# Optimization experiments

Hardware: AMD Instinct MI355X
Metric: run time of the kernel (lower is better)

Reference implementation:

```python
import jax, jax.numpy as jnp
import numpy as np

MAX_RHO = 12.0
N_THETAS = 16
N_RHOS = 5
G = N_THETAS * N_RHOS          # 80 gaussians
W_NUM = 5                      # weights_num == n_feat -> per-channel conv
OUT_DIM = 80                   # conv_shape = [80, 80]
EPS = 1e-5


def _initial_coords():
    grid_rho = np.linspace(0.0, MAX_RHO, num=N_RHOS + 1)[1:]
    grid_theta = np.linspace(0.0, 2.0 * np.pi, num=N_THETAS + 1)[:-1]
    gr, gt = np.meshgrid(grid_rho, grid_theta, sparse=False)
    return gr.T.flatten().astype(np.float32), gt.T.flatten().astype(np.float32)


def setup_inputs() -> dict:
    key = jax.random.key(0)
    ks = jax.random.split(key, 6)
    B, N, V = 2, 500, 64
    input_feat = jax.random.normal(ks[0], (B, N, V, W_NUM), dtype=jnp.float32)
    rho_coords = jax.random.uniform(ks[1], (B, N, V), dtype=jnp.float32) * MAX_RHO
    theta_coords = jax.random.uniform(ks[2], (B, N, V), dtype=jnp.float32) * (2.0 * np.pi)
    mask = (jax.random.uniform(ks[3], (B, N, V, 1)) > 0.2).astype(jnp.float32)

    mu_r0, mu_t0 = _initial_coords()
    mu_rho = jnp.tile(jnp.asarray(mu_r0)[None, :], (W_NUM, 1))       # [W, G]
    mu_theta = jnp.tile(jnp.asarray(mu_t0)[None, :], (W_NUM, 1))     # [W, G]
    sigma_rho = jnp.full((W_NUM, G), MAX_RHO / 8.0, dtype=jnp.float32)
    sigma_theta = jnp.ones((W_NUM, G), dtype=jnp.float32)

    # VarianceScaling(scale=1, fan_avg, uniform): limit = sqrt(3 / fan_avg)
    limit = np.sqrt(3.0 / ((G + OUT_DIM) / 2.0)).astype(np.float32)
    W_conv = jax.random.uniform(ks[4], (W_NUM, G, OUT_DIM), dtype=jnp.float32,
                                minval=-limit, maxval=limit)
    b_conv = jnp.zeros((W_NUM, OUT_DIM), dtype=jnp.float32)

    return {
        "input_feat": input_feat, "rho_coords": rho_coords,
        "theta_coords": theta_coords, "mask": mask,
        "mu_rho": mu_rho, "mu_theta": mu_theta,
        "sigma_rho": sigma_rho, "sigma_theta": sigma_theta,
        "W_conv": W_conv, "b_conv": b_conv,
        "n_rotations": 16,
    }


def reference(input_feat, rho_coords, theta_coords, mask,
              mu_rho, mu_theta, sigma_rho, sigma_theta,
              W_conv, b_conv, n_rotations):
    # input_feat: [B,N,V,W]; rho/theta: [B,N,V]; mask: [B,N,V,1]
    two_pi = 2.0 * np.pi
    # rho gaussian is rotation-independent -> compute once: [B,N,V,W,G]
    g_rho = jnp.exp(-jnp.square(rho_coords[..., None, None] - mu_rho)
                    / (jnp.square(sigma_rho) + EPS))
    m = mask[..., None]                      # [B,N,V,1,1]

    def one_rotation(k):
        th = jnp.mod(theta_coords + k * (two_pi / n_rotations), two_pi)
        g_th = jnp.exp(-jnp.square(th[..., None, None] - mu_theta)
                       / (jnp.square(sigma_theta) + EPS))    # [B,N,V,W,G]
        gauss = g_rho * g_th * m
        gauss = gauss / (jnp.sum(gauss, axis=2, keepdims=True) + EPS)  # mean over vertices
        # weighted patch aggregation: each weight i sees only feature channel i
        desc = jnp.einsum('bnvwg,bnvw->bnwg', gauss, input_feat)
        return jnp.einsum('bnwg,wgo->bnwo', desc, W_conv) + b_conv     # [B,N,W,O]

    ks = jnp.arange(n_rotations, dtype=jnp.float32)

    def body(carry, k):
        return jnp.maximum(carry, one_rotation(k)), None

    init = one_rotation(ks[0])
    out, _ = jax.lax.scan(body, init, ks[1:])
    return out  # [B, n_samples, weights_num, conv_shape[0]]
```

## Files before the change

kernel.cpp:

```cpp
#include <hip/hip_runtime.h>

#define V 64
#define W 5
#define G 80
#define O 80
#define NROT 16
#define GPAD 104
#define EPSV 1e-5f
#define NLOG2E (-1.4426950408889634f)

#define TSTR 72
#define XSTR 68

using bf16x8 = __attribute__((ext_vector_type(8))) short;
using f32x4  = __attribute__((ext_vector_type(4))) float;

__device__ __forceinline__ unsigned short f2bf(float x) {
    unsigned u = __float_as_uint(x);
    unsigned r = (u + 0x7FFFu + ((u >> 16) & 1u)) >> 16;
    return (unsigned short)r;
}
__device__ __forceinline__ float pick5(float a0, float a1, float a2,
                                       float a3, float a4, int r) {
    float x = (r == 1) ? a1 : a0;
    x = (r == 2) ? a2 : x;
    x = (r == 3) ? a3 : x;
    x = (r == 4) ? a4 : x;
    return x;
}

#if __has_builtin(__builtin_amdgcn_mfma_f32_16x16x32_f16)
typedef _Float16 elem_t;
typedef elem_t efrag __attribute__((ext_vector_type(8)));
#define EMFMA(a, b, c) __builtin_amdgcn_mfma_f32_16x16x32_f16((a), (b), (c), 0, 0, 0)
__device__ __forceinline__ unsigned epack(float a, float b) {
    auto r = __builtin_amdgcn_cvt_pkrtz(a, b);
    return __builtin_bit_cast(unsigned, r);
}
#else
typedef short elem_t;
typedef elem_t efrag __attribute__((ext_vector_type(8)));
#define EMFMA(a, b, c) __builtin_amdgcn_mfma_f32_16x16x32_bf16((a), (b), (c), 0, 0, 0)
__device__ __forceinline__ unsigned epack(float a, float b) {
    return (unsigned)f2bf(a) | ((unsigned)f2bf(b) << 16);
}
#endif

__global__ __launch_bounds__(64) void pack_wc_kernel(
    const float* __restrict__ Wc, unsigned short* __restrict__ wsB)
{
    const int f = blockIdx.x, l = threadIdx.x;
    const int w = f / 15, r = f % 15, ks = r / 5, nt = r % 5;
    const int g0 = ks * 32 + ((l >> 4) << 3);
    const int o  = nt * 16 + (l & 15);
    unsigned short v[8];
    #pragma unroll
    for (int i = 0; i < 8; ++i) {
        int g = g0 + i;
        v[i] = (g < G) ? f2bf(Wc[(w * G + g) * O + o]) : (unsigned short)0;
    }
    *(uint4*)(wsB + ((size_t)f * 64 + l) * 8) = *(const uint4*)v;
}

__global__ __launch_bounds__(320, 5) void conv_kernel(
    const float* __restrict__ feat,
    const float* __restrict__ rho,
    const float* __restrict__ theta,
    const float* __restrict__ mask,
    const float* __restrict__ mu_rho,
    const float* __restrict__ mu_theta,
    const float* __restrict__ sig_rho,
    const float* __restrict__ sig_theta,
    const unsigned short* __restrict__ wsB,
    const float* __restrict__ bc,
    float* __restrict__ out)
{
    __shared__ __align__(16) float s_x[NROT][XSTR];
    __shared__ __align__(16) float s_fT[W][XSTR];
    __shared__ __align__(16) float s_arg[5][XSTR];
    __shared__ __align__(16) unsigned short s_A[32 * TSTR];
    __shared__ __align__(16) unsigned short s_descT[W * NROT * GPAD];
    __shared__ float s_red[5][64];
    __shared__ float s_ct[16], s_mt[16], s_sre[8];

    const int tid = threadIdx.x;
    const int p = blockIdx.x;
    const int g = tid % G;
    const int j = tid / G;

    const float kstep = 0.39269908169872414f;
    const float two_pi = 6.283185307179586f;
    const float inv_two_pi = 0.15915494309189535f;

    {
        int v = tid / 5, w = tid - 5 * (tid / 5);
        s_fT[w][v] = feat[p * V * W + tid];
    }
    {
        int r = tid >> 6, v = tid & 63;
        float mu_r = mu_rho[r * 16];
        float sr   = sig_rho[r * 16];
        float c_r  = NLOG2E / (sr * sr + EPSV);
        float rv   = rho[p * V + v];
        float mk   = (mask[p * V + v] != 0.0f) ? 0.0f : -1e30f;
        float dr = rv - mu_r;
        s_arg[r][v] = fmaf(dr * dr, c_r, mk);
    }
    if (tid < 16) {
        float st = sig_theta[tid];
        s_ct[tid] = NLOG2E / (st * st + EPSV);
        s_mt[tid] = mu_theta[tid];
    }
    for (int i = tid; i < V * NROT; i += 320) {
        int v = i >> 4, k = i & 15;
        float x = theta[p * V + v] + (float)k * kstep;
        x -= floorf(x * inv_two_pi) * two_pi;
        s_x[k][v] = x;
    }

    const int wchk = 1 + j;
    const int gr = (g >> 4) << 4;
    const int gt = g & 15;
    int pred = (mu_rho  [wchk * G + g] == mu_rho  [g]) &&
               (mu_theta[wchk * G + g] == mu_theta[g]) &&
               (sig_rho [wchk * G + g] == sig_rho [g]) &&
               (sig_theta[wchk * G + g] == sig_theta[g]) &&
               (mu_rho  [g] == mu_rho  [gr]) &&
               (sig_rho [g] == sig_rho [gr]) &&
               (mu_theta[g] == mu_theta[gt]) &&
               (sig_theta[g] == sig_theta[gt]);
    const int uni = __syncthreads_and(pred);

    if (uni) {
        if (tid < 256) {
            int m = tid >> 3, s = tid & 7;
            unsigned pk0 = 0, pk1 = 0, pk2 = 0, pk3 = 0;
            if (m < 30) {
                int w  = m / 5;
                int rr = (m < 25) ? (m - 5 * w) : (m - 25);
                float mx = -3.0e38f;
                #pragma unroll
                for (int vs = 0; vs < 16; ++vs) {
                    float4 a = *(const float4*)&s_arg[rr][4 * vs];
                    mx = fmaxf(mx, fmaxf(fmaxf(a.x, a.y), fmaxf(a.z, a.w)));
                }
                float sh = fminf(-mx, 60.0f);
                const float* ap = &s_arg[rr][8 * s];
                float4 aa = *(const float4*)ap;
                float4 ab = *(const float4*)(ap + 4);
                float e0 = __builtin_amdgcn_exp2f(aa.x + sh);
                float e1 = __builtin_amdgcn_exp2f(aa.y + sh);
                float e2 = __builtin_amdgcn_exp2f(aa.z + sh);
                float e3 = __builtin_amdgcn_exp2f(aa.w + sh);
                float e4 = __builtin_amdgcn_exp2f(ab.x + sh);
                float e5 = __builtin_amdgcn_exp2f(ab.y + sh);
                float e6 = __builtin_amdgcn_exp2f(ab.z + sh);
                float e7 = __builtin_amdgcn_exp2f(ab.w + sh);
                if (m < 25) {
                    const float* fp = &s_fT[w][8 * s];
                    float4 fa = *(const float4*)fp;
                    float4 fb = *(const float4*)(fp + 4);
                    e0 *= fa.x; e1 *= fa.y; e2 *= fa.z; e3 *= fa.w;
                    e4 *= fb.x; e5 *= fb.y; e6 *= fb.z; e7 *= fb.w;
                }
                pk0 = epack(e0, e1); pk1 = epack(e2, e3);
                pk2 = epack(e4, e5); pk3 = epack(e6, e7);
            }
            *(uint4*)((elem_t*)s_A + m * TSTR + 8 * s) =
                make_uint4(pk0, pk1, pk2, pk3);
        } else if (tid < 261) {
            int r = tid - 256;
            float mx = -3.0e38f;
            #pragma unroll
            for (int vs = 0; vs < 16; ++vs) {
                float4 a = *(const float4*)&s_arg[r][4 * vs];
                mx = fmaxf(mx, fmaxf(fmaxf(a.x, a.y), fmaxf(a.z, a.w)));
            }
            float sh = fminf(-mx, 60.0f);
            s_sre[r] = EPSV * __builtin_amdgcn_exp2f(sh);
        }
        __syncthreads();

        const int ww = tid >> 6;
        const int l  = tid & 63;
        const int lg = l >> 4, lc = l & 15;
        const elem_t* EA = (const elem_t*)s_A;
        efrag a00 = *(const efrag*)(EA + lc * TSTR + (lg << 3));
        efrag a01 = *(const efrag*)(EA + lc * TSTR + 32 + (lg << 3));
        efrag a10 = *(const efrag*)(EA + (16 + lc) * TSTR + (lg << 3));
        efrag a11 = *(const efrag*)(EA + (16 + lc) * TSTR + 32 + (lg << 3));
        const float sre0 = s_sre[0], sre1 = s_sre[1], sre2 = s_sre[2],
                    sre3 = s_sre[3], sre4 = s_sre[4];

        int w0[4], r0[4], w1[4], r1[4];
        bool ok1[4];
        #pragma unroll
        for (int i = 0; i < 4; ++i) {
            int m = lg * 4 + i;
            w0[i] = m / 5; r0[i] = m - 5 * w0[i];
            int m2 = 16 + lg * 4 + i;
            ok1[i] = (m2 < 25);
            int mm = ok1[i] ? m2 : 24;
            w1[i] = mm / 5; r1[i] = mm - 5 * w1[i];
        }

        #pragma unroll
        for (int q = 0; q < 4; ++q) {
            int nt = ww + 5 * q;
            if (nt < 16) {
                float ct = s_ct[nt], mt = s_mt[nt];
                const float* xr = &s_x[lc][lg << 3];
                float4 xa = *(const float4*)(xr);
                float4 xb = *(const float4*)(xr + 4);
                float4 xc = *(const float4*)(xr + 32);
                float4 xd = *(const float4*)(xr + 36);
                float d;
                #define EX(v) (d = (v) - mt, __builtin_amdgcn_exp2f(ct * d * d))
                unsigned u0 = epack(EX(xa.x), EX(xa.y));
                unsigned u1 = epack(EX(xa.z), EX(xa.w));
                unsigned u2 = epack(EX(xb.x), EX(xb.y));
                unsigned u3 = epack(EX(xb.z), EX(xb.w));
                efrag b0 = __builtin_bit_cast(efrag, make_uint4(u0, u1, u2, u3));
                u0 = epack(EX(xc.x), EX(xc.y));
                u1 = epack(EX(xc.z), EX(xc.w));
                u2 = epack(EX(xd.x), EX(xd.y));
                u3 = epack(EX(xd.z), EX(xd.w));
                efrag b1 = __builtin_bit_cast(efrag, make_uint4(u0, u1, u2, u3));
                #undef EX

                f32x4 z = {0.f, 0.f, 0.f, 0.f};
                f32x4 c0 = EMFMA(a00, b0, z);
                c0 = EMFMA(a01, b1, c0);
                f32x4 c1 = EMFMA(a10, b0, z);
                c1 = EMFMA(a11, b1, c1);

                float dn0 = __shfl(c1[1], 32 + lc);
                float dn1 = __shfl(c1[2], 32 + lc);
                float dn2 = __shfl(c1[3], 32 + lc);
                float dn3 = __shfl(c1[0], 48 + lc);
                float dn4 = __shfl(c1[1], 48 + lc);
                float i0 = __builtin_amdgcn_rcpf(dn0 + sre0);
                float i1 = __builtin_amdgcn_rcpf(dn1 + sre1);
                float i2 = __builtin_amdgcn_rcpf(dn2 + sre2);
                float i3 = __builtin_amdgcn_rcpf(dn3 + sre3);
                float i4 = __builtin_amdgcn_rcpf(dn4 + sre4);

                #pragma unroll
                for (int i = 0; i < 4; ++i) {
                    float inv = pick5(i0, i1, i2, i3, i4, r0[i]);
                    s_descT[(w0[i] * 16 + lc) * GPAD + r0[i] * 16 + nt] =
                        f2bf(c0[i] * inv);
                }
                #pragma unroll
                for (int i = 0; i < 4; ++i) {
                    if (ok1[i]) {
                        float inv = pick5(i0, i1, i2, i3, i4, r1[i]);
                        s_descT[(w1[i] * 16 + lc) * GPAD + r1[i] * 16 + nt] =
                            f2bf(c1[i] * inv);
                    }
                }
            }
        }
    } else {
        #pragma unroll 1
        for (int w = 0; w < W; ++w) {
            const float mu_r = mu_rho[w * G + g];
            const float sr   = sig_rho[w * G + g];
            const float c_sr = NLOG2E / (sr * sr + EPSV);
            const float mu_t = mu_theta[w * G + g];
            const float st   = sig_theta[w * G + g];
            const float c_st = NLOG2E / (st * st + EPSV);
            float den[4] = {0.f, 0.f, 0.f, 0.f};
            float nm[4]  = {0.f, 0.f, 0.f, 0.f};
            for (int v = 0; v < V; ++v) {
                float rv  = rho[p * V + v];
                float mk  = (mask[p * V + v] != 0.0f) ? 0.0f : -1e30f;
                float fw  = s_fT[w][v];
                float dr = rv - mu_r;
                float argr = fmaf(dr * dr, c_sr, mk);
                #pragma unroll
                for (int kk = 0; kk < 4; ++kk) {
                    float x = s_x[4 * j + kk][v];
                    float t = x - mu_t;
                    float e = __builtin_amdgcn_exp2f(fmaf(t * t, c_st, argr));
                    den[kk] += e;
                    nm[kk] = fmaf(e, fw, nm[kk]);
                }
            }
            #pragma unroll
            for (int kk = 0; kk < 4; ++kk)
                s_descT[(w * 16 + 4 * j + kk) * GPAD + g] =
                    f2bf(nm[kk] * __builtin_amdgcn_rcpf(den[kk] + EPSV));
        }
    }

    {
        unsigned* d32 = (unsigned*)s_descT;
        for (int i = tid; i < 80 * 12; i += 320)
            d32[(i / 12) * (GPAD / 2) + 40 + (i % 12)] = 0u;
    }
    __syncthreads();

    {
        const int ww = tid >> 6;
        const int l  = tid & 63;
        bf16x8 afrag[3];
        #pragma unroll
        for (int ks = 0; ks < 3; ++ks)
            afrag[ks] = *(const bf16x8*)(s_descT + (ww * 16 + (l & 15)) * GPAD +
                                         ks * 32 + ((l >> 4) << 3));
        #pragma unroll
        for (int nt = 0; nt < 5; ++nt) {
            f32x4 acc = {0.f, 0.f, 0.f, 0.f};
            #pragma unroll
            for (int ks = 0; ks < 3; ++ks) {
                const unsigned short* bp =
                    wsB + ((size_t)(((ww * 3 + ks) * 5 + nt) * 64 + l)) * 8;
                bf16x8 bfrag = *(const bf16x8*)bp;
                acc = __builtin_amdgcn_mfma_f32_16x16x32_bf16(
                          afrag[ks], bfrag, acc, 0, 0, 0);
            }
            float m1 = fmaxf(fmaxf(acc[0], acc[1]), fmaxf(acc[2], acc[3]));
            s_red[ww][l] = m1;
            float r0 = s_red[ww][l & 15];
            float r1 = s_red[ww][(l & 15) + 16];
            float r2 = s_red[ww][(l & 15) + 32];
            float r3 = s_red[ww][(l & 15) + 48];
            float mx = fmaxf(fmaxf(r0, r1), fmaxf(r2, r3));
            if (l < 16) {
                int oo = nt * 16 + l;
                out[p * (W * O) + ww * O + oo] = mx + bc[ww * O + oo];
            }
        }
    }
}

extern "C" void kernel_launch(void* const* d_in, const int* in_sizes, int n_in,
                              void* d_out, int out_size, void* d_ws, size_t ws_size,
                              hipStream_t stream) {
    const float* feat      = (const float*)d_in[0];
    const float* rho       = (const float*)d_in[1];
    const float* theta     = (const float*)d_in[2];
    const float* mask      = (const float*)d_in[3];
    const float* mu_rho    = (const float*)d_in[4];
    const float* mu_theta  = (const float*)d_in[5];
    const float* sig_rho   = (const float*)d_in[6];
    const float* sig_theta = (const float*)d_in[7];
    const float* Wc        = (const float*)d_in[8];
    const float* bc        = (const float*)d_in[9];
    float* outp            = (float*)d_out;

    const int np = in_sizes[1] / V;
    unsigned short* ws = (unsigned short*)d_ws;

    pack_wc_kernel<<<75, 64, 0, stream>>>(Wc, ws);
    conv_kernel<<<np, 320, 0, stream>>>(feat, rho, theta, mask, mu_rho, mu_theta,
                                        sig_rho, sig_theta, ws, bc, outp);
}
```

Baseline: 23.42 us.

## Build MFMA A-fragments in registers, drop s_A staging and one barrier

Each wave now builds its rho-gaussian×feature A fragments directly in registers from s_arg/s_fT, so the s_A shared staging buffer and the __syncthreads after it are gone. The per-rho max shift is computed once with wave shuffles during setup. The theta exponent is expanded into a fused-multiply-add polynomial, and the final max over rows uses xor shuffles instead of the s_red shared round-trip. Occupancy hint is raised from 5 to 6 blocks. The cost is redundant exp2 work, since every wave recomputes the same A fragments. The expanded quadratic may also lose some precision.

Measured after the change: 23.87 us. Within noise of the previous version (+1.9%).

```diff
diff --git a/kernel.cpp b/kernel.cpp
--- a/kernel.cpp
+++ b/kernel.cpp
@@ -9,7 +9,6 @@
 #define EPSV 1e-5f
 #define NLOG2E (-1.4426950408889634f)
 
-#define TSTR 72
 #define XSTR 68
 
 using bf16x8 = __attribute__((ext_vector_type(8))) short;
@@ -62,7 +61,7 @@
     *(uint4*)(wsB + ((size_t)f * 64 + l) * 8) = *(const uint4*)v;
 }
 
-__global__ __launch_bounds__(320, 5) void conv_kernel(
+__global__ __launch_bounds__(320, 6) void conv_kernel(
     const float* __restrict__ feat,
     const float* __restrict__ rho,
     const float* __restrict__ theta,
@@ -78,10 +77,8 @@
     __shared__ __align__(16) float s_x[NROT][XSTR];
     __shared__ __align__(16) float s_fT[W][XSTR];
     __shared__ __align__(16) float s_arg[5][XSTR];
-    __shared__ __align__(16) unsigned short s_A[32 * TSTR];
     __shared__ __align__(16) unsigned short s_descT[W * NROT * GPAD];
-    __shared__ float s_red[5][64];
-    __shared__ float s_ct[16], s_mt[16], s_sre[8];
+    __shared__ float s_ct[16], s_mt[16], s_shift[8], s_sre[8];
 
     const int tid = threadIdx.x;
     const int p = blockIdx.x;
@@ -104,7 +101,20 @@
         float rv   = rho[p * V + v];
         float mk   = (mask[p * V + v] != 0.0f) ? 0.0f : -1e30f;
         float dr = rv - mu_r;
-        s_arg[r][v] = fmaf(dr * dr, c_r, mk);
+        float av = fmaf(dr * dr, c_r, mk);
+        s_arg[r][v] = av;
+        float m = av;
+        m = fmaxf(m, __shfl_xor(m, 1));
+        m = fmaxf(m, __shfl_xor(m, 2));
+        m = fmaxf(m, __shfl_xor(m, 4));
+        m = fmaxf(m, __shfl_xor(m, 8));
+        m = fmaxf(m, __shfl_xor(m, 16));
+        m = fmaxf(m, __shfl_xor(m, 32));
+        if (v == 0) {
+            float sh = fminf(-m, 60.0f);
+            s_shift[r] = sh;
+            s_sre[r]   = EPSV * __builtin_amdgcn_exp2f(sh);
+        }
     }
     if (tid < 16) {
         float st = sig_theta[tid];
@@ -132,63 +142,86 @@
     const int uni = __syncthreads_and(pred);
 
     if (uni) {
-        if (tid < 256) {
-            int m = tid >> 3, s = tid & 7;
-            unsigned pk0 = 0, pk1 = 0, pk2 = 0, pk3 = 0;
-            if (m < 30) {
-                int w  = m / 5;
-                int rr = (m < 25) ? (m - 5 * w) : (m - 25);
-                float mx = -3.0e38f;
-                #pragma unroll
-                for (int vs = 0; vs < 16; ++vs) {
-                    float4 a = *(const float4*)&s_arg[rr][4 * vs];
-                    mx = fmaxf(mx, fmaxf(fmaxf(a.x, a.y), fmaxf(a.z, a.w)));
-                }
-                float sh = fminf(-mx, 60.0f);
-                const float* ap = &s_arg[rr][8 * s];
-                float4 aa = *(const float4*)ap;
-                float4 ab = *(const float4*)(ap + 4);
-                float e0 = __builtin_amdgcn_exp2f(aa.x + sh);
-                float e1 = __builtin_amdgcn_exp2f(aa.y + sh);
-                float e2 = __builtin_amdgcn_exp2f(aa.z + sh);
-                float e3 = __builtin_amdgcn_exp2f(aa.w + sh);
-                float e4 = __builtin_amdgcn_exp2f(ab.x + sh);
-                float e5 = __builtin_amdgcn_exp2f(ab.y + sh);
-                float e6 = __builtin_amdgcn_exp2f(ab.z + sh);
-                float e7 = __builtin_amdgcn_exp2f(ab.w + sh);
-                if (m < 25) {
-                    const float* fp = &s_fT[w][8 * s];
-                    float4 fa = *(const float4*)fp;
-                    float4 fb = *(const float4*)(fp + 4);
-                    e0 *= fa.x; e1 *= fa.y; e2 *= fa.z; e3 *= fa.w;
-                    e4 *= fb.x; e5 *= fb.y; e6 *= fb.z; e7 *= fb.w;
-                }
-                pk0 = epack(e0, e1); pk1 = epack(e2, e3);
-                pk2 = epack(e4, e5); pk3 = epack(e6, e7);
-            }
-            *(uint4*)((elem_t*)s_A + m * TSTR + 8 * s) =
-                make_uint4(pk0, pk1, pk2, pk3);
-        } else if (tid < 261) {
-            int r = tid - 256;
-            float mx = -3.0e38f;
-            #pragma unroll
-            for (int vs = 0; vs < 16; ++vs) {
-                float4 a = *(const float4*)&s_arg[r][4 * vs];
-                mx = fmaxf(mx, fmaxf(fmaxf(a.x, a.y), fmaxf(a.z, a.w)));
-            }
-            float sh = fminf(-mx, 60.0f);
-            s_sre[r] = EPSV * __builtin_amdgcn_exp2f(sh);
-        }
-        __syncthreads();
-
         const int ww = tid >> 6;
         const int l  = tid & 63;
         const int lg = l >> 4, lc = l & 15;
-        const elem_t* EA = (const elem_t*)s_A;
-        efrag a00 = *(const efrag*)(EA + lc * TSTR + (lg << 3));
-        efrag a01 = *(const efrag*)(EA + lc * TSTR + 32 + (lg << 3));
-        efrag a10 = *(const efrag*)(EA + (16 + lc) * TSTR + (lg << 3));
-        efrag a11 = *(const efrag*)(EA + (16 + lc) * TSTR + 32 + (lg << 3));
+        const int v0 = lg << 3;
+
+        efrag a00, a01, a10, a11;
+        {
+            int w_a = lc / 5, r_a = lc - 5 * (lc / 5);
+            float sh = s_shift[r_a];
+            const float* ap = &s_arg[r_a][0];
+            const float* fp = &s_fT[w_a][0];
+            float4 aa = *(const float4*)(ap + v0);
+            float4 ab = *(const float4*)(ap + v0 + 4);
+            float4 fa = *(const float4*)(fp + v0);
+            float4 fb = *(const float4*)(fp + v0 + 4);
+            a00 = __builtin_bit_cast(efrag, make_uint4(
+                epack(__builtin_amdgcn_exp2f(aa.x + sh) * fa.x,
+                      __builtin_amdgcn_exp2f(aa.y + sh) * fa.y),
+                epack(__builtin_amdgcn_exp2f(aa.z + sh) * fa.z,
+                      __builtin_amdgcn_exp2f(aa.w + sh) * fa.w),
+                epack(__builtin_amdgcn_exp2f(ab.x + sh) * fb.x,
+                      __builtin_amdgcn_exp2f(ab.y + sh) * fb.y),
+                epack(__builtin_amdgcn_exp2f(ab.z + sh) * fb.z,
+                      __builtin_amdgcn_exp2f(ab.w + sh) * fb.w)));
+            aa = *(const float4*)(ap + 32 + v0);
+            ab = *(const float4*)(ap + 32 + v0 + 4);
+            fa = *(const float4*)(fp + 32 + v0);
+            fb = *(const float4*)(fp + 32 + v0 + 4);
+            a01 = __builtin_bit_cast(efrag, make_uint4(
+                epack(__builtin_amdgcn_exp2f(aa.x + sh) * fa.x,
+                      __builtin_amdgcn_exp2f(aa.y + sh) * fa.y),
+                epack(__builtin_amdgcn_exp2f(aa.z + sh) * fa.z,
+                      __builtin_amdgcn_exp2f(aa.w + sh) * fa.w),
+                epack(__builtin_amdgcn_exp2f(ab.x + sh) * fb.x,
+                      __builtin_amdgcn_exp2f(ab.y + sh) * fb.y),
+                epack(__builtin_amdgcn_exp2f(ab.z + sh) * fb.z,
+                      __builtin_amdgcn_exp2f(ab.w + sh) * fb.w)));
+        }
+        if (lc < 14) {
+            int m = 16 + lc;
+            bool wf = (m < 25);
+            int w_b = wf ? (m / 5) : 0;
+            int r_b = wf ? (m - 5 * (m / 5)) : (lc - 9);
+            float sh = s_shift[r_b];
+            const float* ap = &s_arg[r_b][0];
+            const float* fp = &s_fT[w_b][0];
+            float4 aa = *(const float4*)(ap + v0);
+            float4 ab = *(const float4*)(ap + v0 + 4);
+            float4 fa = *(const float4*)(fp + v0);
+            float4 fb = *(const float4*)(fp + v0 + 4);
+            if (!wf) { fa = make_float4(1.f,1.f,1.f,1.f); fb = fa; }
+            a10 = __builtin_bit_cast(efrag, make_uint4(
+                epack(__builtin_amdgcn_exp2f(aa.x + sh) * fa.x,
+                      __builtin_amdgcn_exp2f(aa.y + sh) * fa.y),
+                epack(__builtin_amdgcn_exp2f(aa.z + sh) * fa.z,
+                      __builtin_amdgcn_exp2f(aa.w + sh) * fa.w),
+                epack(__builtin_amdgcn_exp2f(ab.x + sh) * fb.x,
+                      __builtin_amdgcn_exp2f(ab.y + sh) * fb.y),
+                epack(__builtin_amdgcn_exp2f(ab.z + sh) * fb.z,
+                      __builtin_amdgcn_exp2f(ab.w + sh) * fb.w)));
+            aa = *(const float4*)(ap + 32 + v0);
+            ab = *(const float4*)(ap + 32 + v0 + 4);
+            fa = *(const float4*)(fp + 32 + v0);
+            fb = *(const float4*)(fp + 32 + v0 + 4);
+            if (!wf) { fa = make_float4(1.f,1.f,1.f,1.f); fb = fa; }
+            a11 = __builtin_bit_cast(efrag, make_uint4(
+                epack(__builtin_amdgcn_exp2f(aa.x + sh) * fa.x,
+                      __builtin_amdgcn_exp2f(aa.y + sh) * fa.y),
+                epack(__builtin_amdgcn_exp2f(aa.z + sh) * fa.z,
+                      __builtin_amdgcn_exp2f(aa.w + sh) * fa.w),
+                epack(__builtin_amdgcn_exp2f(ab.x + sh) * fb.x,
+                      __builtin_amdgcn_exp2f(ab.y + sh) * fb.y),
+                epack(__builtin_amdgcn_exp2f(ab.z + sh) * fb.z,
+                      __builtin_amdgcn_exp2f(ab.w + sh) * fb.w)));
+        } else {
+            uint4 zz = make_uint4(0u, 0u, 0u, 0u);
+            a10 = __builtin_bit_cast(efrag, zz);
+            a11 = __builtin_bit_cast(efrag, zz);
+        }
+
         const float sre0 = s_sre[0], sre1 = s_sre[1], sre2 = s_sre[2],
                     sre3 = s_sre[3], sre4 = s_sre[4];
 
@@ -209,23 +242,21 @@
             int nt = ww + 5 * q;
             if (nt < 16) {
                 float ct = s_ct[nt], mt = s_mt[nt];
-                const float* xr = &s_x[lc][lg << 3];
+                float bco = -2.0f * ct * mt;
+                float cco = ct * mt * mt;
+                const float* xr = &s_x[lc][v0];
                 float4 xa = *(const float4*)(xr);
                 float4 xb = *(const float4*)(xr + 4);
                 float4 xc = *(const float4*)(xr + 32);
                 float4 xd = *(const float4*)(xr + 36);
-                float d;
-                #define EX(v) (d = (v) - mt, __builtin_amdgcn_exp2f(ct * d * d))
-                unsigned u0 = epack(EX(xa.x), EX(xa.y));
-                unsigned u1 = epack(EX(xa.z), EX(xa.w));
-                unsigned u2 = epack(EX(xb.x), EX(xb.y));
-                unsigned u3 = epack(EX(xb.z), EX(xb.w));
-                efrag b0 = __builtin_bit_cast(efrag, make_uint4(u0, u1, u2, u3));
-                u0 = epack(EX(xc.x), EX(xc.y));
-                u1 = epack(EX(xc.z), EX(xc.w));
-                u2 = epack(EX(xd.x), EX(xd.y));
-                u3 = epack(EX(xd.z), EX(xd.w));
-                efrag b1 = __builtin_bit_cast(efrag, make_uint4(u0, u1, u2, u3));
+                #define EX(v) __builtin_amdgcn_exp2f(\
+                    fmaf(fmaf(ct, (v), bco), (v), cco))
+                efrag b0 = __builtin_bit_cast(efrag, make_uint4(
+                    epack(EX(xa.x), EX(xa.y)), epack(EX(xa.z), EX(xa.w)),
+                    epack(EX(xb.x), EX(xb.y)), epack(EX(xb.z), EX(xb.w))));
+                efrag b1 = __builtin_bit_cast(efrag, make_uint4(
+                    epack(EX(xc.x), EX(xc.y)), epack(EX(xc.z), EX(xc.w)),
+                    epack(EX(xd.x), EX(xd.y)), epack(EX(xd.z), EX(xd.w))));
                 #undef EX
 
                 f32x4 z = {0.f, 0.f, 0.f, 0.f};
@@ -321,15 +352,11 @@
                           afrag[ks], bfrag, acc, 0, 0, 0);
             }
             float m1 = fmaxf(fmaxf(acc[0], acc[1]), fmaxf(acc[2], acc[3]));
-            s_red[ww][l] = m1;
-            float r0 = s_red[ww][l & 15];
-            float r1 = s_red[ww][(l & 15) + 16];
-            float r2 = s_red[ww][(l & 15) + 32];
-            float r3 = s_red[ww][(l & 15) + 48];
-            float mx = fmaxf(fmaxf(r0, r1), fmaxf(r2, r3));
+            m1 = fmaxf(m1, __shfl_xor(m1, 16));
+            m1 = fmaxf(m1, __shfl_xor(m1, 32));
             if (l < 16) {
                 int oo = nt * 16 + l;
-                out[p * (W * O) + ww * O + oo] = mx + bc[ww * O + oo];
+                out[p * (W * O) + ww * O + oo] = m1 + bc[ww * O + oo];
             }
         }
     }
```
